# Kernel tuning notes

Hardware: AMD Instinct MI355X
Metric: run time of the kernel (lower is better)

Reference implementation:

```python
import jax, jax.numpy as jnp
import numpy as np

T, B, I, HID = 512, 64, 512, 1024


def setup_inputs() -> dict:
    key = jax.random.key(0)
    k1, k2, k3, k4, k5 = jax.random.split(key, 5)
    scale = 1.0 / np.sqrt(I + HID)
    return {
        "x": jax.random.normal(k1, (T, B, I), dtype=jnp.float32),
        "Wz": jax.random.normal(k2, (HID, I + HID), dtype=jnp.float32) * scale,
        "bz": jax.random.normal(k3, (HID,), dtype=jnp.float32) * scale,
        "Wh": jax.random.normal(k4, (HID, I + HID), dtype=jnp.float32) * scale,
        "bh": jax.random.normal(k5, (HID,), dtype=jnp.float32) * scale,
    }


def reference(x, Wz, bz, Wh, bh):
    # x: [T, B, I]; Wz/Wh: [HID, HID+I] (applied to cat([h, x], axis=1))
    t, b, _ = x.shape
    hid = Wz.shape[0]

    def step(h, xt):
        inp = jnp.concatenate([h, xt], axis=1)          # [B, HID+I]
        g = jax.nn.sigmoid(inp @ Wz.T + bz)             # linear_z
        z = g
        r = g  # faithful to source: r also uses linear_z (linear_r unused)
        cand = jnp.tanh(jnp.concatenate([r * h, xt], axis=1) @ Wh.T + bh)
        h_new = (1.0 - z) * h + z * cand
        return h_new, (h_new, z, r)

    h0 = jnp.zeros((b, hid), dtype=x.dtype)
    _, (Hs, Z, R) = jax.lax.scan(step, h0, x)
    H = jnp.concatenate([h0[None], Hs], axis=0)          # [T+1, B, HID]
    return H, Z, R
```

## Files before the change

### kernel.cpp

```cpp
#include <hip/hip_runtime.h>
#include <cstdint>

typedef unsigned short ushort_t;
typedef __attribute__((ext_vector_type(8))) short short8;
typedef __attribute__((ext_vector_type(4))) float f32x4;
typedef unsigned long long u64;

#define T_STEPS 512
#define BATCH   64
#define IDIM    512
#define HIDDEN  1024
#define NWGP    256
#define BH      (BATCH*HIDDEN)
#define STG     65536
#define SCRR    73728

__device__ __forceinline__ ushort_t f2bf(float f) {
  unsigned int x = __float_as_uint(f);
  unsigned int r = (x + 0x7fffu + ((x >> 16) & 1u)) >> 16;
  return (ushort_t)r;
}
__device__ __forceinline__ float sigmoid_f(float x) { return 1.f / (1.f + __expf(-x)); }
__device__ __forceinline__ float tanh_f(float x)    { return 1.f - 2.f / (1.f + __expf(2.f * x)); }

#define WAITV(N) asm volatile("s_waitcnt vmcnt(" #N ")" ::: "memory")

__device__ __forceinline__ void glds16(const ushort_t* g, ushort_t* l) {
  __builtin_amdgcn_global_load_lds(
      (const __attribute__((address_space(1))) void*)g,
      (__attribute__((address_space(3))) void*)l, 16, 0, 17);
}

#define STAGE4(SRC) do { \
  glds16((SRC),       &smem[stgw]); \
  glds16((SRC) + 64,  &smem[stgw + 512]); \
  glds16((SRC) + 128, &smem[stgw + 1024]); \
  glds16((SRC) + 192, &smem[stgw + 1536]); \
} while (0)

#define KSTEPG(J, VN, WOFF) do { \
  const int k0_ = kqbase + (J) * 32 + koff; \
  short8 b0_ = *(const short8*)&smem[(WOFF) + wb0 + (k0_ ^ sz0)]; \
  short8 b1_ = *(const short8*)&smem[(WOFF) + wb1 + (k0_ ^ sz1)]; \
  WAITV(VN); \
  __builtin_amdgcn_sched_barrier(0); \
  short8 a_ = *(const short8*)&smem[abase + ((J) >> 1) * 512 + (axq ^ (((J) & 1) * 32))]; \
  acc0 = __builtin_amdgcn_mfma_f32_16x16x32_bf16(b0_, a_, acc0, 0, 0, 0); \
  acc1 = __builtin_amdgcn_mfma_f32_16x16x32_bf16(b1_, a_, acc1, 0, 0, 0); \
} while (0)

#define MATVEC8G(WOFF) do { \
  KSTEPG(0,3,WOFF); KSTEPG(1,3,WOFF); KSTEPG(2,2,WOFF); KSTEPG(3,2,WOFF); \
  KSTEPG(4,1,WOFF); KSTEPG(5,1,WOFF); KSTEPG(6,0,WOFF); KSTEPG(7,0,WOFF); \
} while (0)

#define POLL_GRP(TGT) do { \
  if (tid == 0) { \
    while (__hip_atomic_load(gctr, __ATOMIC_RELAXED, __HIP_MEMORY_SCOPE_AGENT) < (TGT)) \
      __builtin_amdgcn_s_sleep(1); \
  } \
  __syncthreads(); \
  WAITV(0); \
  __builtin_amdgcn_sched_barrier(0); \
} while (0)

__global__ __launch_bounds__(256) void convert_weights(
    const float* __restrict__ Wz, const float* __restrict__ Wh,
    ushort_t* __restrict__ Wzh, ushort_t* __restrict__ Wzx,
    ushort_t* __restrict__ Whh, ushort_t* __restrict__ Whx)
{
  int j = blockIdx.x;
  const float* W = blockIdx.y ? Wh : Wz;
  ushort_t* Bh = blockIdx.y ? Whh : Wzh;
  ushort_t* Bx = blockIdx.y ? Whx : Wzx;
  const float* row = W + (size_t)j * (HIDDEN + IDIM);
  for (int c = threadIdx.x; c < HIDDEN + IDIM; c += 256) {
    ushort_t v = f2bf(row[c]);
    if (c < HIDDEN) Bh[(size_t)j * HIDDEN + c] = v;
    else            Bx[(size_t)j * IDIM + (c - HIDDEN)] = v;
  }
}

__global__ __launch_bounds__(256) void gx_gemm2(
    const float* __restrict__ x,
    const ushort_t* __restrict__ Wzx, const ushort_t* __restrict__ Whx,
    const float* __restrict__ bz, const float* __restrict__ bh,
    float* __restrict__ outZ, float* __restrict__ outR)
{
  const int m0 = blockIdx.x * 64;
  const int n0 = blockIdx.y * 64;
  __shared__ ushort_t As[64 * 40];
  __shared__ ushort_t Bzs[64 * 40];
  __shared__ ushort_t Bhs[64 * 40];
  const int tid = threadIdx.x;
  const int lane = tid & 63, w4 = tid >> 6;
  const int row = tid >> 2, q = tid & 3;
  f32x4 accz[4] = {{0,0,0,0},{0,0,0,0},{0,0,0,0},{0,0,0,0}};
  f32x4 acch[4] = {{0,0,0,0},{0,0,0,0},{0,0,0,0},{0,0,0,0}};
  for (int kk = 0; kk < IDIM; kk += 32) {
    const float* xs = &x[(size_t)(m0 + row) * IDIM + kk + q * 8];
    float4 f0 = *(const float4*)xs;
    float4 f1 = *(const float4*)(xs + 4);
    short8 av;
    av[0]=f2bf(f0.x); av[1]=f2bf(f0.y); av[2]=f2bf(f0.z); av[3]=f2bf(f0.w);
    av[4]=f2bf(f1.x); av[5]=f2bf(f1.y); av[6]=f2bf(f1.z); av[7]=f2bf(f1.w);
    short8 bzv = *(const short8*)&Wzx[(size_t)(n0 + row) * IDIM + kk + q * 8];
    short8 bhv = *(const short8*)&Whx[(size_t)(n0 + row) * IDIM + kk + q * 8];
    __syncthreads();
    *(short8*)&As[row * 40 + q * 8]  = av;
    *(short8*)&Bzs[row * 40 + q * 8] = bzv;
    *(short8*)&Bhs[row * 40 + q * 8] = bhv;
    __syncthreads();
    short8 af = *(const short8*)&As[(w4 * 16 + (lane & 15)) * 40 + (lane >> 4) * 8];
    #pragma unroll
    for (int c = 0; c < 4; ++c) {
      short8 bzf = *(const short8*)&Bzs[(c * 16 + (lane & 15)) * 40 + (lane >> 4) * 8];
      short8 bhf = *(const short8*)&Bhs[(c * 16 + (lane & 15)) * 40 + (lane >> 4) * 8];
      accz[c] = __builtin_amdgcn_mfma_f32_16x16x32_bf16(af, bzf, accz[c], 0, 0, 0);
      acch[c] = __builtin_amdgcn_mfma_f32_16x16x32_bf16(af, bhf, acch[c], 0, 0, 0);
    }
  }
  #pragma unroll
  for (int c = 0; c < 4; ++c) {
    int j = n0 + c * 16 + (lane & 15);
    float bzv = bz[j], bhv = bh[j];
    #pragma unroll
    for (int r = 0; r < 4; ++r) {
      int m = m0 + w4 * 16 + (lane >> 4) * 4 + r;
      outZ[(size_t)m * HIDDEN + j] = accz[c][r] + bzv;
      outR[(size_t)m * HIDDEN + j] = acch[c][r] + bhv;
    }
  }
}

__global__ __launch_bounds__(256) void gru_persist(
    const ushort_t* __restrict__ Wzh, const ushort_t* __restrict__ Whh,
    float* __restrict__ H, float* __restrict__ Z, float* __restrict__ R,
    u64* __restrict__ h_buf, u64* __restrict__ ghb, int* __restrict__ ctrs)
{
  extern __shared__ ushort_t smem[];
  const int tid = threadIdx.x;
  const int lane = tid & 63, wv = tid >> 6;
  const int grp = blockIdx.x & 7, slot = blockIdx.x >> 3;
  const int rbase = grp * 8;
  const int jbase = slot * 32;
  int* gctr = ctrs + grp * 32;
  const ushort_t* hgu = (const ushort_t*)h_buf;
  const ushort_t* ggu = (const ushort_t*)ghb;

  for (int c = tid; c < 32 * 128; c += 256) {
    int row = c >> 7, k8 = (c & 127) * 8;
    int dst = row * 1024 + (k8 ^ ((row & 7) << 3));
    *(short8*)&smem[dst]         = *(const short8*)&Wzh[(size_t)(jbase + row) * 1024 + k8];
    *(short8*)&smem[32768 + dst] = *(const short8*)&Whh[(size_t)(jbase + row) * 1024 + k8];
  }
  __syncthreads();

  if (tid < 64) {
    float4 z4 = {0.f, 0.f, 0.f, 0.f};
    *(float4*)&H[(size_t)(rbase + (tid >> 3)) * 1024 + jbase + (tid & 7) * 4] = z4;
  }

  const int li = lane & 15, q4 = lane >> 4;
  const int kqbase = wv * 256;
  const int koff = q4 * 8;
  const int wb0 = li * 1024,     wb1 = (16 + li) * 1024;
  const int sz0 = (li & 7) << 3, sz1 = ((16 + li) & 7) << 3;
  const int srow = lane >> 3, schk = (lane & 7) ^ srow;
  const ushort_t* srcAh = hgu + (size_t)(rbase + srow) * 1024 + kqbase + schk * 8;
  const ushort_t* srcAg = ggu + (size_t)(rbase + srow) * 1024 + kqbase + schk * 8;
  const int stgw = STG + wv * 2048;
  const int abase = stgw + (li & 7) * 64;
  const int axq = (q4 ^ (li & 7)) * 8;
  const bool epi = (wv < 2) && (li < 8);
  const int erow = rbase + li;
  const int ecol = jbase + (wv & 1) * 16 + q4 * 4;
  const int gidx = (erow * 1024 + ecol) >> 2;
  const int rr0 = SCRR + ((0 * 4 + wv) * 64 + lane) * 8;
  const int rr1 = SCRR + ((1 * 4 + wv) * 64 + lane) * 8;
  const int rrc = SCRR + ((wv & 1) * 4 * 64 + lane) * 8;

  float hreg[4] = {0.f, 0.f, 0.f, 0.f};
  float g[4], hn[4], gz[4], gh[4];

  for (int t = 0; t < T_STEPS; ++t) {
    const size_t zoff = (size_t)t * BH;

    if (epi) {
      f32x4 z4 = *(const f32x4*)&Z[zoff + (size_t)erow * 1024 + ecol];
      f32x4 r4 = *(const f32x4*)&R[zoff + (size_t)erow * 1024 + ecol];
      #pragma unroll
      for (int r = 0; r < 4; ++r) { gz[r] = z4[r]; gh[r] = r4[r]; }
    }

    POLL_GRP(64 * t);

    f32x4 acc0 = {0, 0, 0, 0}, acc1 = {0, 0, 0, 0};
    STAGE4(srcAh);
    MATVEC8G(0);

    *(f32x4*)&smem[rr0] = acc0;
    *(f32x4*)&smem[rr1] = acc1;
    __syncthreads();
    if (epi) {
      f32x4 s = *(const f32x4*)&smem[rrc];
      #pragma unroll
      for (int q = 1; q < 4; ++q) {
        f32x4 o = *(const f32x4*)&smem[rrc + q * 64 * 8];
        #pragma unroll
        for (int r = 0; r < 4; ++r) s[r] += o[r];
      }
      #pragma unroll
      for (int r = 0; r < 4; ++r) g[r] = sigmoid_f(s[r] + gz[r]);
      u64 v = (u64)f2bf(g[0] * hreg[0])
            | ((u64)f2bf(g[1] * hreg[1]) << 16)
            | ((u64)f2bf(g[2] * hreg[2]) << 32)
            | ((u64)f2bf(g[3] * hreg[3]) << 48);
      __hip_atomic_store(ghb + gidx, v, __ATOMIC_RELAXED, __HIP_MEMORY_SCOPE_AGENT);
    }
    WAITV(0);
    __syncthreads();
    if (tid == 0)
      __hip_atomic_fetch_add(gctr, 1, __ATOMIC_RELAXED, __HIP_MEMORY_SCOPE_AGENT);

    POLL_GRP(64 * t + 32);

    acc0 = (f32x4){0, 0, 0, 0}; acc1 = (f32x4){0, 0, 0, 0};
    STAGE4(srcAg);
    MATVEC8G(32768);

    *(f32x4*)&smem[rr0] = acc0;
    *(f32x4*)&smem[rr1] = acc1;
    __syncthreads();
    if (epi) {
      f32x4 s = *(const f32x4*)&smem[rrc];
      #pragma unroll
      for (int q = 1; q < 4; ++q) {
        f32x4 o = *(const f32x4*)&smem[rrc + q * 64 * 8];
        #pragma unroll
        for (int r = 0; r < 4; ++r) s[r] += o[r];
      }
      #pragma unroll
      for (int r = 0; r < 4; ++r) {
        float cand = tanh_f(s[r] + gh[r]);
        hn[r] = (1.f - g[r]) * hreg[r] + g[r] * cand;
        hreg[r] = hn[r];
      }
      u64 v = (u64)f2bf(hn[0])
            | ((u64)f2bf(hn[1]) << 16)
            | ((u64)f2bf(hn[2]) << 32)
            | ((u64)f2bf(hn[3]) << 48);
      __hip_atomic_store(h_buf + gidx, v, __ATOMIC_RELAXED, __HIP_MEMORY_SCOPE_AGENT);
    }
    WAITV(0);
    __syncthreads();
    if (tid == 0)
      __hip_atomic_fetch_add(gctr, 1, __ATOMIC_RELAXED, __HIP_MEMORY_SCOPE_AGENT);

    if (epi) {
      const size_t hoff = (size_t)(t + 1) * BH;
      const size_t rowo = (size_t)erow * 1024 + ecol;
      float4 gv = {g[0], g[1], g[2], g[3]};
      float4 hv = {hn[0], hn[1], hn[2], hn[3]};
      *(float4*)&Z[zoff + rowo] = gv;
      *(float4*)&R[zoff + rowo] = gv;
      *(float4*)&H[hoff + rowo] = hv;
    }
  }
}

extern "C" void kernel_launch(void* const* d_in, const int* in_sizes, int n_in,
                              void* d_out, int out_size, void* d_ws, size_t ws_size,
                              hipStream_t stream) {
  (void)in_sizes; (void)n_in; (void)out_size; (void)ws_size;
  const float* x  = (const float*)d_in[0];
  const float* Wz = (const float*)d_in[1];
  const float* bz = (const float*)d_in[2];
  const float* Wh = (const float*)d_in[3];
  const float* bh = (const float*)d_in[4];

  float* H = (float*)d_out;
  float* Z = H + (size_t)(T_STEPS + 1) * BH;
  float* R = Z + (size_t)T_STEPS * BH;

  char* ws = (char*)d_ws;
  int*      ctrs  = (int*)ws;
  u64*      h_buf = (u64*)(ws + 16384);
  u64*      ghb   = (u64*)(ws + 16384 + 131072);
  ushort_t* Wzh   = (ushort_t*)(ws + 16384 + 2 * 131072);
  ushort_t* Whh   = Wzh + (size_t)HIDDEN * HIDDEN;
  ushort_t* Wzx   = Whh + (size_t)HIDDEN * HIDDEN;
  ushort_t* Whx   = Wzx + (size_t)HIDDEN * IDIM;

  hipFuncSetAttribute((const void*)gru_persist,
                      hipFuncAttributeMaxDynamicSharedMemorySize, 155648);

  hipMemsetAsync(ctrs, 0, 16384, stream);
  hipMemsetAsync(h_buf, 0, 131072, stream);
  convert_weights<<<dim3(HIDDEN, 2), 256, 0, stream>>>(Wz, Wh, Wzh, Wzx, Whh, Whx);
  gx_gemm2<<<dim3(T_STEPS * BATCH / 64, HIDDEN / 64), 256, 0, stream>>>(
      x, Wzx, Whx, bz, bh, Z, R);
  gru_persist<<<NWGP, 256, 155648, stream>>>(Wzh, Whh, H, Z, R, h_buf, ghb, ctrs);
}
```

Measured before the change: 2.346 ms.

## Prefetch next-step gate inputs in persistent loop and widen gx GEMM tile

Moves the per-step global loads of the precomputed Z/R gate inputs off the critical path. Each step now issues the next step's loads after publishing h, and relaxes the memory wait so those loads stay in flight across the barrier. The input GEMM also widens its N tile to 128 columns so each converted x tile is reused across more outputs. This adds register pressure in the GEMM and relies on the vmcnt ordering to keep the h_buf store visible before the counter increment.

```diff
diff --git a/kernel.cpp b/kernel.cpp
--- a/kernel.cpp
+++ b/kernel.cpp
@@ -88,15 +88,17 @@
     float* __restrict__ outZ, float* __restrict__ outR)
 {
   const int m0 = blockIdx.x * 64;
-  const int n0 = blockIdx.y * 64;
+  const int n0 = blockIdx.y * 128;
   __shared__ ushort_t As[64 * 40];
-  __shared__ ushort_t Bzs[64 * 40];
-  __shared__ ushort_t Bhs[64 * 40];
+  __shared__ ushort_t Bzs[128 * 40];
+  __shared__ ushort_t Bhs[128 * 40];
   const int tid = threadIdx.x;
   const int lane = tid & 63, w4 = tid >> 6;
+  const int li = lane & 15, q4 = lane >> 4;
   const int row = tid >> 2, q = tid & 3;
-  f32x4 accz[4] = {{0,0,0,0},{0,0,0,0},{0,0,0,0},{0,0,0,0}};
-  f32x4 acch[4] = {{0,0,0,0},{0,0,0,0},{0,0,0,0},{0,0,0,0}};
+  f32x4 accz[8], acch[8];
+  #pragma unroll
+  for (int c = 0; c < 8; ++c) { accz[c] = (f32x4){0,0,0,0}; acch[c] = (f32x4){0,0,0,0}; }
   for (int kk = 0; kk < IDIM; kk += 32) {
     const float* xs = &x[(size_t)(m0 + row) * IDIM + kk + q * 8];
     float4 f0 = *(const float4*)xs;
@@ -104,29 +106,33 @@
     short8 av;
     av[0]=f2bf(f0.x); av[1]=f2bf(f0.y); av[2]=f2bf(f0.z); av[3]=f2bf(f0.w);
     av[4]=f2bf(f1.x); av[5]=f2bf(f1.y); av[6]=f2bf(f1.z); av[7]=f2bf(f1.w);
-    short8 bzv = *(const short8*)&Wzx[(size_t)(n0 + row) * IDIM + kk + q * 8];
-    short8 bhv = *(const short8*)&Whx[(size_t)(n0 + row) * IDIM + kk + q * 8];
-    __syncthreads();
-    *(short8*)&As[row * 40 + q * 8]  = av;
-    *(short8*)&Bzs[row * 40 + q * 8] = bzv;
-    *(short8*)&Bhs[row * 40 + q * 8] = bhv;
-    __syncthreads();
-    short8 af = *(const short8*)&As[(w4 * 16 + (lane & 15)) * 40 + (lane >> 4) * 8];
+    short8 bz0 = *(const short8*)&Wzx[(size_t)(n0 + row) * IDIM + kk + q * 8];
+    short8 bz1 = *(const short8*)&Wzx[(size_t)(n0 + 64 + row) * IDIM + kk + q * 8];
+    short8 bh0 = *(const short8*)&Whx[(size_t)(n0 + row) * IDIM + kk + q * 8];
+    short8 bh1 = *(const short8*)&Whx[(size_t)(n0 + 64 + row) * IDIM + kk + q * 8];
+    __syncthreads();
+    *(short8*)&As[row * 40 + q * 8]         = av;
+    *(short8*)&Bzs[row * 40 + q * 8]        = bz0;
+    *(short8*)&Bzs[(64 + row) * 40 + q * 8] = bz1;
+    *(short8*)&Bhs[row * 40 + q * 8]        = bh0;
+    *(short8*)&Bhs[(64 + row) * 40 + q * 8] = bh1;
+    __syncthreads();
+    short8 af = *(const short8*)&As[(w4 * 16 + li) * 40 + q4 * 8];
     #pragma unroll
-    for (int c = 0; c < 4; ++c) {
-      short8 bzf = *(const short8*)&Bzs[(c * 16 + (lane & 15)) * 40 + (lane >> 4) * 8];
-      short8 bhf = *(const short8*)&Bhs[(c * 16 + (lane & 15)) * 40 + (lane >> 4) * 8];
+    for (int c = 0; c < 8; ++c) {
+      short8 bzf = *(const short8*)&Bzs[(c * 16 + li) * 40 + q4 * 8];
+      short8 bhf = *(const short8*)&Bhs[(c * 16 + li) * 40 + q4 * 8];
       accz[c] = __builtin_amdgcn_mfma_f32_16x16x32_bf16(af, bzf, accz[c], 0, 0, 0);
       acch[c] = __builtin_amdgcn_mfma_f32_16x16x32_bf16(af, bhf, acch[c], 0, 0, 0);
     }
   }
   #pragma unroll
-  for (int c = 0; c < 4; ++c) {
-    int j = n0 + c * 16 + (lane & 15);
+  for (int c = 0; c < 8; ++c) {
+    int j = n0 + c * 16 + li;
     float bzv = bz[j], bhv = bh[j];
     #pragma unroll
     for (int r = 0; r < 4; ++r) {
-      int m = m0 + w4 * 16 + (lane >> 4) * 4 + r;
+      int m = m0 + w4 * 16 + q4 * 4 + r;
       outZ[(size_t)m * HIDDEN + j] = accz[c][r] + bzv;
       outR[(size_t)m * HIDDEN + j] = acch[c][r] + bhv;
     }
@@ -183,15 +189,15 @@
   float hreg[4] = {0.f, 0.f, 0.f, 0.f};
   float g[4], hn[4], gz[4], gh[4];
 
+  if (epi) {
+    f32x4 z4 = *(const f32x4*)&Z[(size_t)erow * 1024 + ecol];
+    f32x4 r4 = *(const f32x4*)&R[(size_t)erow * 1024 + ecol];
+    #pragma unroll
+    for (int r = 0; r < 4; ++r) { gz[r] = z4[r]; gh[r] = r4[r]; }
+  }
+
   for (int t = 0; t < T_STEPS; ++t) {
     const size_t zoff = (size_t)t * BH;
-
-    if (epi) {
-      f32x4 z4 = *(const f32x4*)&Z[zoff + (size_t)erow * 1024 + ecol];
-      f32x4 r4 = *(const f32x4*)&R[zoff + (size_t)erow * 1024 + ecol];
-      #pragma unroll
-      for (int r = 0; r < 4; ++r) { gz[r] = z4[r]; gh[r] = r4[r]; }
-    }
 
     POLL_GRP(64 * t);
 
@@ -251,8 +257,13 @@
             | ((u64)f2bf(hn[2]) << 32)
             | ((u64)f2bf(hn[3]) << 48);
       __hip_atomic_store(h_buf + gidx, v, __ATOMIC_RELAXED, __HIP_MEMORY_SCOPE_AGENT);
-    }
-    WAITV(0);
+      const size_t pnoff = (size_t)((t + 1) & (T_STEPS - 1)) * BH;
+      f32x4 z4 = *(const f32x4*)&Z[pnoff + (size_t)erow * 1024 + ecol];
+      f32x4 r4 = *(const f32x4*)&R[pnoff + (size_t)erow * 1024 + ecol];
+      #pragma unroll
+      for (int r = 0; r < 4; ++r) { gz[r] = z4[r]; gh[r] = r4[r]; }
+    }
+    WAITV(2);
     __syncthreads();
     if (tid == 0)
       __hip_atomic_fetch_add(gctr, 1, __ATOMIC_RELAXED, __HIP_MEMORY_SCOPE_AGENT);
@@ -298,7 +309,7 @@
   hipMemsetAsync(ctrs, 0, 16384, stream);
   hipMemsetAsync(h_buf, 0, 131072, stream);
   convert_weights<<<dim3(HIDDEN, 2), 256, 0, stream>>>(Wz, Wh, Wzh, Wzx, Whh, Whx);
-  gx_gemm2<<<dim3(T_STEPS * BATCH / 64, HIDDEN / 64), 256, 0, stream>>>(
+  gx_gemm2<<<dim3(T_STEPS * BATCH / 64, HIDDEN / 128), 256, 0, stream>>>(
       x, Wzx, Whx, bz, bh, Z, R);
   gru_persist<<<NWGP, 256, 155648, stream>>>(Wzh, Whh, H, Z, R, h_buf, ghb, ctrs);
 }
```

Result: slower. 2.724 ms (+16.1%).
